# Performance work log

Hardware: AMD Instinct MI355X
Metric: run time of the kernel (lower is better)

## Reference

```python
import jax, jax.numpy as jnp
import numpy as np

EMBED_DIM = 768
D_K = 64
B, S = 4, 4096


def setup_inputs() -> dict:
    key = jax.random.key(0)
    ks = jax.random.split(key, 7)
    scale = 1.0 / np.sqrt(EMBED_DIM)
    return {
        "x": jax.random.normal(ks[0], (B, S, EMBED_DIM), dtype=jnp.float32),
        "Wq": jax.random.normal(ks[1], (EMBED_DIM, D_K), dtype=jnp.float32) * scale,
        "bq": jax.random.normal(ks[2], (D_K,), dtype=jnp.float32) * 0.01,
        "Wk": jax.random.normal(ks[3], (EMBED_DIM, D_K), dtype=jnp.float32) * scale,
        "bk": jax.random.normal(ks[4], (D_K,), dtype=jnp.float32) * 0.01,
        "Wv": jax.random.normal(ks[5], (EMBED_DIM, D_K), dtype=jnp.float32) * scale,
        "bv": jax.random.normal(ks[6], (D_K,), dtype=jnp.float32) * 0.01,
    }


def reference(x, Wq, bq, Wk, bk, Wv, bv):
    # Linear projections: [B, S, E] @ [E, d_k] + bias -> [B, S, d_k]
    q = jnp.einsum("bse,ed->bsd", x, Wq) + bq
    k = jnp.einsum("bse,ed->bsd", x, Wk) + bk
    v = jnp.einsum("bse,ed->bsd", x, Wv) + bv
    # Scaled dot-product attention; scores: [B, S, S]
    scores = jnp.einsum("bqd,bkd->bqk", q, k) / jnp.sqrt(jnp.asarray(D_K, x.dtype))
    attn = jax.nn.softmax(scores, axis=-1)
    return jnp.einsum("bqk,bkd->bqd", attn, v)
```

## Files before the change

### kernel.cpp

```cpp
#include <hip/hip_runtime.h>

typedef _Float16 f16;
typedef f16 f16x2 __attribute__((ext_vector_type(2)));
typedef f16 f16x4 __attribute__((ext_vector_type(4)));
typedef f16 f16x8 __attribute__((ext_vector_type(8)));
typedef float f32x4 __attribute__((ext_vector_type(4)));
typedef float f32x16 __attribute__((ext_vector_type(16)));

#define MFMA32(A, B, C) __builtin_amdgcn_mfma_f32_16x16x32_f16(A, B, C, 0, 0, 0)
#define MFMAKK(A, B, C) __builtin_amdgcn_mfma_f32_32x32x16_f16(A, B, C, 0, 0, 0)

#define QSCALE (0.125f * 1.44269504088896340736f)
#define MSHIFT 10.0f

__device__ __forceinline__ f16x2 pkrtz(float a, float b) {
  return __builtin_bit_cast(f16x2, __builtin_amdgcn_cvt_pkrtz(a, b));
}
__device__ __forceinline__ void nts(f16* p, f16x8 v) {
  __builtin_nontemporal_store(v, (f16x8*)p);
}
__device__ __forceinline__ f16x8 ntl(const f16* p) {
  return __builtin_nontemporal_load((const f16x8*)p);
}

__global__ __launch_bounds__(256) void wtrans_kernel(
    const float* __restrict__ Wq, const float* __restrict__ Wk,
    const float* __restrict__ Wv, f16* __restrict__ Wt) {
  __shared__ float T[64][65];
  const int t = threadIdx.x;
  const int kt = blockIdx.x;
  const int z = blockIdx.y;
  const float* W = (z == 0) ? Wq : ((z == 1) ? Wk : Wv);

  {
    const int kl = t >> 2, c0 = (t & 3) * 16;
    const float* wp = W + (kt * 64 + kl) * 64 + c0;
    float4 v0 = *(const float4*)wp;
    float4 v1 = *(const float4*)(wp + 4);
    float4 v2 = *(const float4*)(wp + 8);
    float4 v3 = *(const float4*)(wp + 12);
    float* Tr = &T[kl][c0];
    Tr[0] = v0.x; Tr[1] = v0.y; Tr[2] = v0.z; Tr[3] = v0.w;
    Tr[4] = v1.x; Tr[5] = v1.y; Tr[6] = v1.z; Tr[7] = v1.w;
    Tr[8] = v2.x; Tr[9] = v2.y; Tr[10] = v2.z; Tr[11] = v2.w;
    Tr[12] = v3.x; Tr[13] = v3.y; Tr[14] = v3.z; Tr[15] = v3.w;
  }
  __syncthreads();
  {
    const int n = t >> 2, k0 = (t & 3) * 16;
    union { f16x2 h2[8]; f16x8 h8[2]; } u;
#pragma unroll
    for (int i = 0; i < 8; i++)
      u.h2[i] = pkrtz(T[k0 + 2 * i][n], T[k0 + 2 * i + 1][n]);
    f16* dst = Wt + (z * 64 + n) * 768 + kt * 64 + k0;
    *(f16x8*)dst = u.h8[0];
    *(f16x8*)(dst + 8) = u.h8[1];
  }
}

__global__ __launch_bounds__(256, 4) void proj_kernel(
    const float* __restrict__ x, const f16* __restrict__ Wt,
    const float* __restrict__ bq, const float* __restrict__ bk,
    const float* __restrict__ bv, f16* __restrict__ qo, f16* __restrict__ ko,
    f16* __restrict__ vt) {
  __shared__ f16 Xs[32][72];
  __shared__ f16 Ws[192][72];

  const int t = threadIdx.x;
  const int w = t >> 6;
  const int lane = t & 63;
  const int ln = lane & 15;
  const int quad = lane >> 4;
  const int mh = w & 1;
  const int nh = w >> 1;
  const int r0 = blockIdx.x * 32;

  f32x4 acc[6];
#pragma unroll
  for (int i = 0; i < 6; i++) acc[i] = (f32x4){0.f, 0.f, 0.f, 0.f};

  const int xsr = t >> 3, xsc = (t & 7) * 8;
  const int wsr = t >> 2, wsc = (t & 3) * 16;
  const float* xr = x + (r0 + xsr) * 768 + xsc;
  const f16* wr = Wt + wsr * 768 + wsc;

  float4 xa0, xa1;
  f16x8 wf[3][2];
  xa0 = *(const float4*)xr;
  xa1 = *(const float4*)(xr + 4);
#pragma unroll
  for (int p = 0; p < 3; p++) {
    wf[p][0] = *(const f16x8*)(wr + p * 64 * 768);
    wf[p][1] = *(const f16x8*)(wr + p * 64 * 768 + 8);
  }

  for (int kc = 0; kc < 12; kc++) {
    __syncthreads();
    {
      union { f16x2 h2[4]; f16x8 h8; } u;
      u.h2[0] = pkrtz(xa0.x, xa0.y); u.h2[1] = pkrtz(xa0.z, xa0.w);
      u.h2[2] = pkrtz(xa1.x, xa1.y); u.h2[3] = pkrtz(xa1.z, xa1.w);
      *(f16x8*)&Xs[xsr][xsc] = u.h8;
#pragma unroll
      for (int p = 0; p < 3; p++) {
        *(f16x8*)&Ws[p * 64 + wsr][wsc] = wf[p][0];
        *(f16x8*)&Ws[p * 64 + wsr][wsc + 8] = wf[p][1];
      }
    }
    if (kc + 1 < 12) {
      const float* xp = xr + (kc + 1) * 64;
      xa0 = *(const float4*)xp;
      xa1 = *(const float4*)(xp + 4);
      const f16* wp = wr + (kc + 1) * 64;
#pragma unroll
      for (int p = 0; p < 3; p++) {
        wf[p][0] = *(const f16x8*)(wp + p * 64 * 768);
        wf[p][1] = *(const f16x8*)(wp + p * 64 * 768 + 8);
      }
    }
    __syncthreads();

    f16x8 a0 = *(const f16x8*)&Xs[mh * 16 + ln][quad * 8];
    f16x8 a1 = *(const f16x8*)&Xs[mh * 16 + ln][32 + quad * 8];
#pragma unroll
    for (int nt = 0; nt < 6; nt++) {
      f16x8 b0 = *(const f16x8*)&Ws[nh * 96 + nt * 16 + ln][quad * 8];
      f16x8 b1 = *(const f16x8*)&Ws[nh * 96 + nt * 16 + ln][32 + quad * 8];
      acc[nt] = MFMA32(a0, b0, acc[nt]);
      acc[nt] = MFMA32(a1, b1, acc[nt]);
    }
  }

  const int rowg = r0 + mh * 16 + quad * 4;
  if (nh == 0) {
#pragma unroll
    for (int nt = 0; nt < 4; nt++) {
      int d = nt * 16 + ln;
      float bb = bq[d];
#pragma unroll
      for (int r = 0; r < 4; r++)
        qo[(rowg + r) * 64 + d] = (f16)((acc[nt][r] + bb) * QSCALE);
    }
#pragma unroll
    for (int nt = 4; nt < 6; nt++) {
      int d = nt * 16 + ln - 64;
      float bb = bk[d];
#pragma unroll
      for (int r = 0; r < 4; r++)
        ko[(rowg + r) * 64 + d] = (f16)(acc[nt][r] + bb);
    }
  } else {
#pragma unroll
    for (int nt = 0; nt < 2; nt++) {
      int d = 32 + nt * 16 + ln;
      float bb = bk[d];
#pragma unroll
      for (int r = 0; r < 4; r++)
        ko[(rowg + r) * 64 + d] = (f16)(acc[nt][r] + bb);
    }
    const int bidx = rowg >> 12;
    const int sb = rowg & 4095;
#pragma unroll
    for (int nt = 2; nt < 6; nt++) {
      int dv = nt * 16 + ln - 32;
      float bb = bv[dv];
      f16x4 hv;
#pragma unroll
      for (int r = 0; r < 4; r++) hv[r] = (f16)(acc[nt][r] + bb);
      *(f16x4*)&vt[((bidx * 64 + dv) << 12) + sb] = hv;
    }
  }
}

__global__ __launch_bounds__(512, 4) void attn_kernel(
    const f16* __restrict__ qo, const f16* __restrict__ ko,
    const f16* __restrict__ vt, f16* __restrict__ po, float* __restrict__ pl) {
  constexpr int NK = 512;
  __shared__ f16 Ksh[2][64][76];
  __shared__ f16 Vsh[2][64][76];

  const int t = threadIdx.x;
  const int w = t >> 6;
  const int lane = t & 63;
  const int l32 = lane & 31;
  const int hh = lane >> 5;
  const int bid = blockIdx.x;
  const int c = bid & 7;
  const int qb = bid >> 3;
  const int b = qb >> 4;
  const int g = qb * 8 + w;

  f16x8 qf[4];
  {
    const f16* qp = qo + (size_t)(qb * 256 + w * 32 + l32) * 64 + hh * 8;
#pragma unroll
    for (int dblk = 0; dblk < 4; dblk++)
      qf[dblk] = *(const f16x8*)(qp + dblk * 16);
  }

  f32x16 o0, o1;
#pragma unroll
  for (int r = 0; r < 16; r++) { o0[r] = 0.f; o1[r] = 0.f; }
  float l_s = 0.f;

  const int rr = t >> 3;
  const int cc = (t & 7) * 8;
  const f16* kbase = ko + (b * 4096 + c * NK) * 64;
  const f16* vbase = vt + b * 64 * 4096 + c * NK;

  f16x8 kreg = *(const f16x8*)(kbase + rr * 64 + cc);
  f16x8 vreg = *(const f16x8*)(vbase + rr * 4096 + cc);
  *(f16x8*)&Ksh[0][rr][cc] = kreg;
  *(f16x8*)&Vsh[0][rr][cc] = vreg;

#pragma unroll 1
  for (int kt = 0; kt < NK / 64; kt++) {
    const int cur = kt & 1;
    if (kt + 1 < NK / 64) {
      const int ks1 = (kt + 1) * 64;
      kreg = *(const f16x8*)(kbase + (ks1 + rr) * 64 + cc);
      vreg = *(const f16x8*)(vbase + rr * 4096 + ks1 + cc);
    }
    __syncthreads();

    const f16(*Kc)[76] = Ksh[cur];
    const f16(*Vc)[76] = Vsh[cur];

#pragma unroll 1
    for (int kblk = 0; kblk < 2; kblk++) {
      f32x16 st;
#pragma unroll
      for (int r = 0; r < 16; r++) st[r] = -MSHIFT;
#pragma unroll
      for (int dblk = 0; dblk < 4; dblk++) {
        union { f16x4 q4[2]; f16x8 h; } ka;
        const f16* kp = &Kc[kblk * 32 + l32][dblk * 16 + hh * 8];
        ka.q4[0] = *(const f16x4*)(kp);
        ka.q4[1] = *(const f16x4*)(kp + 4);
        st = MFMAKK(ka.h, qf[dblk], st);
      }
#pragma unroll
      for (int r = 0; r < 16; r++) {
        st[r] = __builtin_amdgcn_exp2f(st[r]);
        l_s += st[r];
      }
      union { f16x2 h2[8]; f16x8 h8[2]; } pu;
#pragma unroll
      for (int j = 0; j < 8; j++) pu.h2[j] = pkrtz(st[2 * j], st[2 * j + 1]);

#pragma unroll
      for (int nt = 0; nt < 2; nt++) {
        const int kc = kblk * 32 + nt * 16 + 4 * hh;
        union { f16x4 q4[2]; f16x8 h; } vb0, vb1;
        vb0.q4[0] = *(const f16x4*)&Vc[l32][kc];
        vb0.q4[1] = *(const f16x4*)&Vc[l32][kc + 8];
        vb1.q4[0] = *(const f16x4*)&Vc[32 + l32][kc];
        vb1.q4[1] = *(const f16x4*)&Vc[32 + l32][kc + 8];
        o0 = MFMAKK(pu.h8[nt], vb0.h, o0);
        o1 = MFMAKK(pu.h8[nt], vb1.h, o1);
      }
    }

    if (kt + 1 < NK / 64) {
      *(f16x8*)&Ksh[cur ^ 1][rr][cc] = kreg;
      *(f16x8*)&Vsh[cur ^ 1][rr][cc] = vreg;
    }
  }

  union { f16x2 h2[8]; f16x8 h8[2]; } ua, ub;
#pragma unroll
  for (int j = 0; j < 8; j++) {
    ua.h2[j] = pkrtz(o0[2 * j], o0[2 * j + 1]);
    ub.h2[j] = pkrtz(o1[2 * j], o1[2 * j + 1]);
  }
  f16* p = po + ((size_t)(c * 512 + g) * 64 + lane) * 32;
  nts(p, ua.h8[0]);
  nts(p + 8, ua.h8[1]);
  nts(p + 16, ub.h8[0]);
  nts(p + 24, ub.h8[1]);
  float rs = l_s + __shfl_xor(l_s, 32);
  if (hh == 0) pl[c * 16384 + g * 32 + l32] = rs;
}

__global__ __launch_bounds__(256) void merge_kernel(
    const f16* __restrict__ po, const float* __restrict__ pl,
    float* __restrict__ out) {
  __shared__ float inv_sh[4][32];
  const int t = threadIdx.x;
  const int w = t >> 6;
  const int lane = t & 63;
  const int l32 = lane & 31;
  const int hh = lane >> 5;
  const int g = blockIdx.x * 4 + w;

  if (hh == 0) {
    float den = 0.f;
#pragma unroll
    for (int c = 0; c < 8; c++) den += pl[c * 16384 + g * 32 + l32];
    inv_sh[w][l32] = 1.0f / den;
  }

  float o2a[16], o2b[16];
#pragma unroll
  for (int r = 0; r < 16; r++) { o2a[r] = 0.f; o2b[r] = 0.f; }
#pragma unroll
  for (int c = 0; c < 8; c++) {
    const f16* p = po + ((size_t)(c * 512 + g) * 64 + lane) * 32;
    f16x8 l0 = ntl(p);
    f16x8 l1 = ntl(p + 8);
    f16x8 l2 = ntl(p + 16);
    f16x8 l3 = ntl(p + 24);
#pragma unroll
    for (int r = 0; r < 8; r++) {
      o2a[r] += (float)l0[r];
      o2a[r + 8] += (float)l1[r];
      o2b[r] += (float)l2[r];
      o2b[r + 8] += (float)l3[r];
    }
  }
  __syncthreads();
#pragma unroll
  for (int r = 0; r < 16; r++) {
    const int q = (r & 3) + 8 * (r >> 2) + 4 * hh;
    const float inv = inv_sh[w][q];
    float* orow = out + (size_t)(g * 32 + q) * 64 + l32;
    orow[0] = o2a[r] * inv;
    orow[32] = o2b[r] * inv;
  }
}

extern "C" void kernel_launch(void* const* d_in, const int* in_sizes, int n_in,
                              void* d_out, int out_size, void* d_ws,
                              size_t ws_size, hipStream_t stream) {
  const float* x = (const float*)d_in[0];
  const float* Wq = (const float*)d_in[1];
  const float* bq = (const float*)d_in[2];
  const float* Wk = (const float*)d_in[3];
  const float* bk = (const float*)d_in[4];
  const float* Wv = (const float*)d_in[5];
  const float* bv = (const float*)d_in[6];
  float* out = (float*)d_out;

  char* ws = (char*)d_ws;
  f16* Wt = (f16*)ws;
  f16* qo = (f16*)(ws + 294912);
  f16* ko = (f16*)(ws + 294912 + 2097152);
  f16* vt = (f16*)(ws + 294912 + 2 * 2097152);
  const size_t base = 6586368;

  f16* po = (f16*)(ws + base);
  float* pl = (float*)(ws + base + (size_t)8 * 512 * 64 * 32 * 2);

  wtrans_kernel<<<dim3(12, 3), dim3(256), 0, stream>>>(Wq, Wk, Wv, Wt);
  proj_kernel<<<dim3(512), dim3(256), 0, stream>>>(x, Wt, bq, bk, bv, qo, ko, vt);
  attn_kernel<<<dim3(512), dim3(512), 0, stream>>>(qo, ko, vt, po, pl);
  merge_kernel<<<dim3(128), dim3(256), 0, stream>>>(po, pl, out);
}
```

Before: 143.1 us.

## Fuse split-K merge into attention kernel via per-group atomic completion counter

Removes the separate merge kernel launch. Each warp in the attention kernel now bumps an atomic counter for its query group after writing its partial output and row sum. The last of the eight key-chunk contributors reduces all partials and writes the final normalized output. Counters are zeroed in the weight-transpose kernel. This saves a launch and its tail, at the cost of extra fences and atomics and a serialized reduction tail inside the attention kernel.

```diff
diff --git a/kernel.cpp b/kernel.cpp
--- a/kernel.cpp
+++ b/kernel.cpp
@@ -25,11 +25,16 @@
 
 __global__ __launch_bounds__(256) void wtrans_kernel(
     const float* __restrict__ Wq, const float* __restrict__ Wk,
-    const float* __restrict__ Wv, f16* __restrict__ Wt) {
+    const float* __restrict__ Wv, f16* __restrict__ Wt,
+    unsigned* __restrict__ cnt) {
   __shared__ float T[64][65];
   const int t = threadIdx.x;
   const int kt = blockIdx.x;
   const int z = blockIdx.y;
+  if (kt == 0 && z == 0) {
+    cnt[t] = 0u;
+    cnt[t + 256] = 0u;
+  }
   const float* W = (z == 0) ? Wq : ((z == 1) ? Wk : Wv);
 
   {
@@ -174,7 +179,8 @@
 
 __global__ __launch_bounds__(512, 4) void attn_kernel(
     const f16* __restrict__ qo, const f16* __restrict__ ko,
-    const f16* __restrict__ vt, f16* __restrict__ po, float* __restrict__ pl) {
+    const f16* __restrict__ vt, f16* __restrict__ po, float* __restrict__ pl,
+    unsigned* __restrict__ cnt, float* __restrict__ out) {
   constexpr int NK = 512;
   __shared__ f16 Ksh[2][64][76];
   __shared__ f16 Vsh[2][64][76];
@@ -279,53 +285,47 @@
   nts(p + 16, ub.h8[0]);
   nts(p + 24, ub.h8[1]);
   float rs = l_s + __shfl_xor(l_s, 32);
-  if (hh == 0) pl[c * 16384 + g * 32 + l32] = rs;
-}
-
-__global__ __launch_bounds__(256) void merge_kernel(
-    const f16* __restrict__ po, const float* __restrict__ pl,
-    float* __restrict__ out) {
-  __shared__ float inv_sh[4][32];
-  const int t = threadIdx.x;
-  const int w = t >> 6;
-  const int lane = t & 63;
-  const int l32 = lane & 31;
-  const int hh = lane >> 5;
-  const int g = blockIdx.x * 4 + w;
-
-  if (hh == 0) {
+  if (hh == 0)
+    __builtin_nontemporal_store(rs, &pl[c * 16384 + g * 32 + l32]);
+
+  __threadfence();
+  unsigned old = 0;
+  if (lane == 0) old = atomicAdd(&cnt[g], 1u);
+  old = __shfl(old, 0);
+  if (old == 7u) {
+    __threadfence();
     float den = 0.f;
 #pragma unroll
-    for (int c = 0; c < 8; c++) den += pl[c * 16384 + g * 32 + l32];
-    inv_sh[w][l32] = 1.0f / den;
-  }
-
-  float o2a[16], o2b[16];
-#pragma unroll
-  for (int r = 0; r < 16; r++) { o2a[r] = 0.f; o2b[r] = 0.f; }
-#pragma unroll
-  for (int c = 0; c < 8; c++) {
-    const f16* p = po + ((size_t)(c * 512 + g) * 64 + lane) * 32;
-    f16x8 l0 = ntl(p);
-    f16x8 l1 = ntl(p + 8);
-    f16x8 l2 = ntl(p + 16);
-    f16x8 l3 = ntl(p + 24);
-#pragma unroll
-    for (int r = 0; r < 8; r++) {
-      o2a[r] += (float)l0[r];
-      o2a[r + 8] += (float)l1[r];
-      o2b[r] += (float)l2[r];
-      o2b[r + 8] += (float)l3[r];
-    }
-  }
-  __syncthreads();
-#pragma unroll
-  for (int r = 0; r < 16; r++) {
-    const int q = (r & 3) + 8 * (r >> 2) + 4 * hh;
-    const float inv = inv_sh[w][q];
-    float* orow = out + (size_t)(g * 32 + q) * 64 + l32;
-    orow[0] = o2a[r] * inv;
-    orow[32] = o2b[r] * inv;
+    for (int c2 = 0; c2 < 8; c2++)
+      den += __builtin_nontemporal_load(&pl[c2 * 16384 + g * 32 + l32]);
+    const float inv = 1.0f / den;
+
+    float o2a[16], o2b[16];
+#pragma unroll
+    for (int r = 0; r < 16; r++) { o2a[r] = 0.f; o2b[r] = 0.f; }
+#pragma unroll
+    for (int c2 = 0; c2 < 8; c2++) {
+      const f16* p2 = po + ((size_t)(c2 * 512 + g) * 64 + lane) * 32;
+      f16x8 l0 = ntl(p2);
+      f16x8 l1 = ntl(p2 + 8);
+      f16x8 l2 = ntl(p2 + 16);
+      f16x8 l3 = ntl(p2 + 24);
+#pragma unroll
+      for (int r = 0; r < 8; r++) {
+        o2a[r] += (float)l0[r];
+        o2a[r + 8] += (float)l1[r];
+        o2b[r] += (float)l2[r];
+        o2b[r + 8] += (float)l3[r];
+      }
+    }
+#pragma unroll
+    for (int r = 0; r < 16; r++) {
+      const int q = (r & 3) + 8 * (r >> 2) + 4 * hh;
+      const float iv = __shfl(inv, q);
+      float* orow = out + (size_t)(g * 32 + q) * 64 + l32;
+      orow[0] = o2a[r] * iv;
+      orow[32] = o2b[r] * iv;
+    }
   }
 }
 
@@ -350,9 +350,10 @@
 
   f16* po = (f16*)(ws + base);
   float* pl = (float*)(ws + base + (size_t)8 * 512 * 64 * 32 * 2);
-
-  wtrans_kernel<<<dim3(12, 3), dim3(256), 0, stream>>>(Wq, Wk, Wv, Wt);
+  unsigned* cnt = (unsigned*)(ws + base + (size_t)8 * 512 * 64 * 32 * 2 +
+                              524288);
+
+  wtrans_kernel<<<dim3(12, 3), dim3(256), 0, stream>>>(Wq, Wk, Wv, Wt, cnt);
   proj_kernel<<<dim3(512), dim3(256), 0, stream>>>(x, Wt, bq, bk, bv, qo, ko, vt);
-  attn_kernel<<<dim3(512), dim3(512), 0, stream>>>(qo, ko, vt, po, pl);
-  merge_kernel<<<dim3(128), dim3(256), 0, stream>>>(po, pl, out);
-}
+  attn_kernel<<<dim3(512), dim3(512), 0, stream>>>(qo, ko, vt, po, pl, cnt, out);
+}
```

Measured after the change: 395.3 us. +176.2%, slower.
